# Performance work log

Measured on AMD Instinct MI355X. Metric: run time of the kernel, lower is better.

The kernel has to match this reference:

```python
import jax, jax.numpy as jnp
import numpy as np

CROSS_NUM, EXPERT_NUM, LOW_RANK = 3, 4, 64
BATCH, DIM = 32768, 512


def setup_inputs() -> dict:
    key = jax.random.key(0)
    ks = jax.random.split(key, 6)
    s = 0.05  # small init so tanh stays in its linear-ish range
    return {
        "x": jax.random.normal(ks[0], (BATCH, DIM), dtype=jnp.float32),
        "Vs": jax.random.normal(ks[1], (CROSS_NUM, EXPERT_NUM, LOW_RANK, DIM), dtype=jnp.float32) * s,
        "Cs": jax.random.normal(ks[2], (CROSS_NUM, EXPERT_NUM, LOW_RANK, LOW_RANK), dtype=jnp.float32) * s,
        "Us": jax.random.normal(ks[3], (CROSS_NUM, EXPERT_NUM, DIM, LOW_RANK), dtype=jnp.float32) * s,
        "bias": jax.random.normal(ks[4], (CROSS_NUM, DIM), dtype=jnp.float32) * s,
        "gate_w": jax.random.normal(ks[5], (DIM, EXPERT_NUM), dtype=jnp.float32) * s,
    }


def reference(x, Vs, Cs, Us, bias, gate_w):
    # x: [B, D]. The original keeps a trailing singleton axis; we drop it and
    # batch the per-expert einsum chain over the expert axis e.
    x0 = x
    x_l = x
    for i in range(CROSS_NUM):
        # gating (shared Dense(1) per expert, applied to current x_l): [B, E]
        g = x_l @ gate_w
        # low-rank expert chain, batched over experts
        v = jnp.tanh(jnp.einsum('eld,bd->bel', Vs[i], x_l))   # [B, E, low]
        c = jnp.tanh(jnp.einsum('elk,bek->bel', Cs[i], v))    # [B, E, low]
        u = jnp.einsum('edl,bel->bed', Us[i], c)              # [B, E, D]
        expert_out = (u + bias[i][None, None, :]) * x0[:, None, :]  # [B, E, D]
        # mixture combine (raw gating scores, no softmax, as in original)
        moe = jnp.einsum('bed,be->bd', expert_out, g)
        x_l = moe + x_l
    return x_l
```

## Files before the change

### kernel.cpp

```cpp
#include <hip/hip_runtime.h>
#include <hip/hip_bf16.h>


#define CROSS   3
#define ENUM    4
#define LR      64
#define ELD     256
#define DIM     512
#define BATCH   32768
#define BT      32
#define MT      2
#define NTHR    512

#define XL_W    520
#define Y_W     264

typedef __bf16 bf16x8 __attribute__((ext_vector_type(8)));
typedef float  f32x4  __attribute__((ext_vector_type(4)));
typedef unsigned short us;
typedef unsigned short us4 __attribute__((ext_vector_type(4)));

__device__ __forceinline__ us f2bf(float f) {
    return __builtin_bit_cast(us, (__bf16)f);
}
__device__ __forceinline__ float bf2f(us b) {
    unsigned int u = ((unsigned int)b) << 16;
    return __builtin_bit_cast(float, u);
}
__device__ __forceinline__ float tanh_fast(float x) {
    float t = __expf(2.f * x);
    return (t - 1.f) * __builtin_amdgcn_rcpf(t + 1.f);
}

#define MFMA(a, b, c) __builtin_amdgcn_mfma_f32_16x16x32_bf16(a, b, c, 0, 0, 0)

__global__ __launch_bounds__(64) void swz_all(
    const float* __restrict__ Vs, const float* __restrict__ Cs,
    const float* __restrict__ Us, const float* __restrict__ gw,
    us* __restrict__ Vf, us* __restrict__ Cf,
    us* __restrict__ Uf, us* __restrict__ Gf)
{
    int b = blockIdx.x;
    int lane = threadIdx.x;
    if (b < 768) {
        int i = b >> 8, t = b & 255;
        int nt = t >> 4, ks = t & 15;
        int n  = nt * 16 + (lane & 15);
        int k0 = ks * 32 + (lane >> 4) * 8;
        const float* src = Vs + (size_t)i * ELD * DIM + (size_t)n * DIM + k0;
        us* dst = Vf + (size_t)i * ELD * DIM
                + ((size_t)(nt * 16 + ks) * 64 + lane) * 8;
        #pragma unroll
        for (int j = 0; j < 8; ++j) dst[j] = f2bf(src[j]);
    } else if (b < 1536) {
        int bb = b - 768;
        int i = bb >> 8, t = bb & 255;
        int nt = t >> 3, ks = t & 7;
        int n  = nt * 16 + (lane & 15);
        int k0 = ks * 32 + (lane >> 4) * 8;
        int e = k0 >> 6, l0 = k0 & 63;
        const float* src = Us + (size_t)i * ENUM * DIM * LR
                         + (size_t)e * DIM * LR + (size_t)n * LR + l0;
        us* dst = Uf + (size_t)i * DIM * ELD
                + ((size_t)(nt * 8 + ks) * 64 + lane) * 8;
        #pragma unroll
        for (int j = 0; j < 8; ++j) dst[j] = f2bf(src[j]);
    } else if (b < 1632) {
        int bb = b - 1536;
        int i = bb >> 5, rest = bb & 31;
        int e = rest >> 3, t = rest & 7;
        int nt = t >> 1, ks = t & 1;
        int n  = nt * 16 + (lane & 15);
        int k0 = ks * 32 + (lane >> 4) * 8;
        const float* src = Cs + (((size_t)(i * ENUM + e) * LR + n) * LR) + k0;
        us* dst = Cf + (size_t)i * ENUM * LR * LR
                + ((size_t)((e * 4 + nt) * 2 + ks) * 64 + lane) * 8;
        #pragma unroll
        for (int j = 0; j < 8; ++j) dst[j] = f2bf(src[j]);
    } else {
        int ks = b - 1632;
        int n  = lane & 15;
        int k0 = ks * 32 + (lane >> 4) * 8;
        us* dst = Gf + ((size_t)ks * 64 + lane) * 8;
        #pragma unroll
        for (int j = 0; j < 8; ++j)
            dst[j] = (n < ENUM) ? f2bf(gw[(size_t)(k0 + j) * ENUM + n]) : (us)0;
    }
}

__global__ __launch_bounds__(NTHR, 6) void dcn_fused(
    const float* __restrict__ x,
    float* __restrict__ out,
    const us* __restrict__ Vf,
    const us* __restrict__ Cf,
    const us* __restrict__ Uf,
    const us* __restrict__ Gf,
    const float* __restrict__ bias)
{
    __shared__ us xl_s[BT * XL_W];
    __shared__ us y_s[BT * Y_W];
    __shared__ float g_s[BT * ENUM];

    const int tid  = threadIdx.x;
    const int wave = tid >> 6, lane = tid & 63;
    const int quad = lane >> 4, nl = lane & 15;
    const int row0 = blockIdx.x * BT;

    #pragma unroll
    for (int it = 0; it < 8; ++it) {
        int f4 = tid + it * NTHR;
        int r = f4 >> 7, c4 = f4 & 127;
        float4 v = *reinterpret_cast<const float4*>(
            x + (size_t)(row0 + r) * DIM + c4 * 4);
        us4 p;
        p[0] = f2bf(v.x); p[1] = f2bf(v.y); p[2] = f2bf(v.z); p[3] = f2bf(v.w);
        *reinterpret_cast<us4*>(&xl_s[r * XL_W + c4 * 4]) = p;
    }
    __syncthreads();

    unsigned int x0p[MT][4][2];
    #pragma unroll
    for (int mt = 0; mt < MT; ++mt)
        #pragma unroll
        for (int nt = 0; nt < 4; ++nt) {
            int rb = mt * 16 + quad * 4;
            int col = wave * 64 + nt * 16 + nl;
            unsigned int b0 = xl_s[(rb + 0) * XL_W + col];
            unsigned int b1 = xl_s[(rb + 1) * XL_W + col];
            unsigned int b2 = xl_s[(rb + 2) * XL_W + col];
            unsigned int b3 = xl_s[(rb + 3) * XL_W + col];
            x0p[mt][nt][0] = b0 | (b1 << 16);
            x0p[mt][nt][1] = b2 | (b3 << 16);
        }

    #pragma unroll 1
    for (int layer = 0; layer < CROSS; ++layer) {
        const us* Vl = Vf + (size_t)layer * ELD * DIM;
        const us* Cl = Cf + (size_t)layer * ENUM * LR * LR;
        const us* Ul = Uf + (size_t)layer * DIM * ELD;
        const float* bl = bias + layer * DIM;

        f32x4 acc1[MT][2];
        f32x4 gacc[MT];
        #pragma unroll
        for (int mt = 0; mt < MT; ++mt) {
            gacc[mt] = (f32x4)0.f;
            acc1[mt][0] = (f32x4)0.f;
            acc1[mt][1] = (f32x4)0.f;
        }
        #pragma unroll 4
        for (int ks = 0; ks < 16; ++ks) {
            bf16x8 a[MT];
            #pragma unroll
            for (int mt = 0; mt < MT; ++mt)
                a[mt] = *reinterpret_cast<const bf16x8*>(
                    &xl_s[(mt * 16 + nl) * XL_W + ks * 32 + quad * 8]);
            #pragma unroll
            for (int nt = 0; nt < 2; ++nt) {
                bf16x8 bfr = *reinterpret_cast<const bf16x8*>(
                    &Vl[((size_t)((wave * 2 + nt) * 16 + ks) * 64 + lane) * 8]);
                #pragma unroll
                for (int mt = 0; mt < MT; ++mt)
                    acc1[mt][nt] = MFMA(a[mt], bfr, acc1[mt][nt]);
            }
            if (wave == 0) {
                bf16x8 bg = *reinterpret_cast<const bf16x8*>(
                    &Gf[((size_t)ks * 64 + lane) * 8]);
                #pragma unroll
                for (int mt = 0; mt < MT; ++mt)
                    gacc[mt] = MFMA(a[mt], bg, gacc[mt]);
            }
        }
        #pragma unroll
        for (int mt = 0; mt < MT; ++mt)
            #pragma unroll
            for (int r = 0; r < 4; ++r) {
                int row = mt * 16 + quad * 4 + r;
                #pragma unroll
                for (int nt = 0; nt < 2; ++nt)
                    y_s[row * Y_W + wave * 32 + nt * 16 + nl] =
                        f2bf(tanh_fast(acc1[mt][nt][r]));
            }
        if (wave == 0 && nl < ENUM) {
            #pragma unroll
            for (int mt = 0; mt < MT; ++mt)
                #pragma unroll
                for (int r = 0; r < 4; ++r)
                    g_s[(mt * 16 + quad * 4 + r) * ENUM + nl] = gacc[mt][r];
        }
        __syncthreads();

        const int e = wave >> 1, h = wave & 1;
        f32x4 acc2[MT][2];
        #pragma unroll
        for (int mt = 0; mt < MT; ++mt) {
            acc2[mt][0] = (f32x4)0.f;
            acc2[mt][1] = (f32x4)0.f;
        }
        #pragma unroll
        for (int ks = 0; ks < 2; ++ks) {
            bf16x8 a[MT];
            #pragma unroll
            for (int mt = 0; mt < MT; ++mt)
                a[mt] = *reinterpret_cast<const bf16x8*>(
                    &y_s[(mt * 16 + nl) * Y_W + e * 64 + ks * 32 + quad * 8]);
            #pragma unroll
            for (int nt = 0; nt < 2; ++nt) {
                bf16x8 bfr = *reinterpret_cast<const bf16x8*>(
                    &Cl[((size_t)((e * 4 + h * 2 + nt) * 2 + ks) * 64 + lane) * 8]);
                #pragma unroll
                for (int mt = 0; mt < MT; ++mt)
                    acc2[mt][nt] = MFMA(a[mt], bfr, acc2[mt][nt]);
            }
        }
        __syncthreads();
        #pragma unroll
        for (int mt = 0; mt < MT; ++mt)
            #pragma unroll
            for (int r = 0; r < 4; ++r) {
                int row = mt * 16 + quad * 4 + r;
                float gv = g_s[row * ENUM + e];
                #pragma unroll
                for (int nt = 0; nt < 2; ++nt)
                    y_s[row * Y_W + e * 64 + h * 32 + nt * 16 + nl] =
                        f2bf(tanh_fast(acc2[mt][nt][r]) * gv);
            }
        __syncthreads();

        float Gv[MT][4];
        #pragma unroll
        for (int mt = 0; mt < MT; ++mt)
            #pragma unroll
            for (int r = 0; r < 4; ++r) {
                int row = mt * 16 + quad * 4 + r;
                f32x4 g4 = *reinterpret_cast<const f32x4*>(&g_s[row * ENUM]);
                Gv[mt][r] = g4[0] + g4[1] + g4[2] + g4[3];
            }

        #pragma unroll 1
        for (int h3 = 0; h3 < 2; ++h3) {
            float bc[2];
            bc[0] = bl[wave * 64 + h3 * 32 + nl];
            bc[1] = bl[wave * 64 + h3 * 32 + 16 + nl];
            f32x4 acc3[MT][2];
            #pragma unroll
            for (int mt = 0; mt < MT; ++mt) {
                acc3[mt][0] = (f32x4)0.f;
                acc3[mt][1] = (f32x4)0.f;
            }
            #pragma unroll 2
            for (int ks = 0; ks < 8; ++ks) {
                bf16x8 a[MT];
                #pragma unroll
                for (int mt = 0; mt < MT; ++mt)
                    a[mt] = *reinterpret_cast<const bf16x8*>(
                        &y_s[(mt * 16 + nl) * Y_W + ks * 32 + quad * 8]);
                #pragma unroll
                for (int nt = 0; nt < 2; ++nt) {
                    bf16x8 bfr = *reinterpret_cast<const bf16x8*>(
                        &Ul[((size_t)((wave * 4 + h3 * 2 + nt) * 8 + ks) * 64
                             + lane) * 8]);
                    #pragma unroll
                    for (int mt = 0; mt < MT; ++mt)
                        acc3[mt][nt] = MFMA(a[mt], bfr, acc3[mt][nt]);
                }
            }

            #pragma unroll
            for (int nt = 0; nt < 2; ++nt) {
                int col = wave * 64 + h3 * 32 + nt * 16 + nl;
                #pragma unroll
                for (int mt = 0; mt < MT; ++mt)
                    #pragma unroll
                    for (int r = 0; r < 4; ++r) {
                        int row = mt * 16 + quad * 4 + r;
                        float x0v = bf2f((us)(
                            x0p[mt][h3 * 2 + nt][r >> 1] >> ((r & 1) * 16)));
                        float xlo = bf2f(xl_s[row * XL_W + col]);
                        float res = xlo
                                  + x0v * (acc3[mt][nt][r] + bc[nt] * Gv[mt][r]);
                        if (layer == CROSS - 1)
                            out[(size_t)(row0 + row) * DIM + col] = res;
                        else
                            xl_s[row * XL_W + col] = f2bf(res);
                    }
            }
        }
        if (layer < CROSS - 1) __syncthreads();
    }
}

extern "C" void kernel_launch(void* const* d_in, const int* in_sizes, int n_in,
                              void* d_out, int out_size, void* d_ws,
                              size_t ws_size, hipStream_t stream) {
    const float* x      = (const float*)d_in[0];
    const float* Vs     = (const float*)d_in[1];
    const float* Cs     = (const float*)d_in[2];
    const float* Us     = (const float*)d_in[3];
    const float* bias   = (const float*)d_in[4];
    const float* gate_w = (const float*)d_in[5];
    float* out = (float*)d_out;

    us* Vf = (us*)d_ws;
    us* Uf = Vf + (size_t)CROSS * ELD * DIM;
    us* Cf = Uf + (size_t)CROSS * DIM * ELD;
    us* Gf = Cf + (size_t)CROSS * ENUM * LR * LR;

    swz_all<<<1648, 64, 0, stream>>>(Vs, Cs, Us, gate_w, Vf, Cf, Uf, Gf);
    dcn_fused<<<BATCH / BT, NTHR, 0, stream>>>(x, out, Vf, Cf, Uf, Gf, bias);
}
```

Baseline: 334.6 us.

## Double-buffer expert activations to drop a barrier and widen U-GEMM tile

Adds a second LDS buffer so the tanh(C·v)·g results go to z_s instead of overwriting y_s, which removes one __syncthreads between the C-GEMM reads and the writes. The U-projection loop is restructured so each wave computes all four 16-column tiles in a single pass with full unrolling, instead of two halves. The layer-1 K loop unroll is also raised. The wider accumulator set and extra LDS lower the occupancy hint from 6 to 4 waves per EU and may add register pressure.

```diff
diff --git a/kernel.cpp b/kernel.cpp
--- a/kernel.cpp
+++ b/kernel.cpp
@@ -88,7 +88,7 @@
     }
 }
 
-__global__ __launch_bounds__(NTHR, 6) void dcn_fused(
+__global__ __launch_bounds__(NTHR, 4) void dcn_fused(
     const float* __restrict__ x,
     float* __restrict__ out,
     const us* __restrict__ Vf,
@@ -99,6 +99,7 @@
 {
     __shared__ us xl_s[BT * XL_W];
     __shared__ us y_s[BT * Y_W];
+    __shared__ us z_s[BT * Y_W];
     __shared__ float g_s[BT * ENUM];
 
     const int tid  = threadIdx.x;
@@ -148,7 +149,7 @@
             acc1[mt][0] = (f32x4)0.f;
             acc1[mt][1] = (f32x4)0.f;
         }
-        #pragma unroll 4
+        #pragma unroll 8
         for (int ks = 0; ks < 16; ++ks) {
             bf16x8 a[MT];
             #pragma unroll
@@ -213,7 +214,6 @@
                     acc2[mt][nt] = MFMA(a[mt], bfr, acc2[mt][nt]);
             }
         }
-        __syncthreads();
         #pragma unroll
         for (int mt = 0; mt < MT; ++mt)
             #pragma unroll
@@ -222,7 +222,7 @@
                 float gv = g_s[row * ENUM + e];
                 #pragma unroll
                 for (int nt = 0; nt < 2; ++nt)
-                    y_s[row * Y_W + e * 64 + h * 32 + nt * 16 + nl] =
+                    z_s[row * Y_W + e * 64 + h * 32 + nt * 16 + nl] =
                         f2bf(tanh_fast(acc2[mt][nt][r]) * gv);
             }
         __syncthreads();
@@ -237,54 +237,47 @@
                 Gv[mt][r] = g4[0] + g4[1] + g4[2] + g4[3];
             }
 
-        #pragma unroll 1
-        for (int h3 = 0; h3 < 2; ++h3) {
-            float bc[2];
-            bc[0] = bl[wave * 64 + h3 * 32 + nl];
-            bc[1] = bl[wave * 64 + h3 * 32 + 16 + nl];
-            f32x4 acc3[MT][2];
-            #pragma unroll
-            for (int mt = 0; mt < MT; ++mt) {
-                acc3[mt][0] = (f32x4)0.f;
-                acc3[mt][1] = (f32x4)0.f;
-            }
-            #pragma unroll 2
-            for (int ks = 0; ks < 8; ++ks) {
-                bf16x8 a[MT];
+        f32x4 acc3[MT][4];
+        #pragma unroll
+        for (int mt = 0; mt < MT; ++mt)
+            #pragma unroll
+            for (int nt = 0; nt < 4; ++nt) acc3[mt][nt] = (f32x4)0.f;
+        #pragma unroll
+        for (int ks = 0; ks < 8; ++ks) {
+            bf16x8 a[MT];
+            #pragma unroll
+            for (int mt = 0; mt < MT; ++mt)
+                a[mt] = *reinterpret_cast<const bf16x8*>(
+                    &z_s[(mt * 16 + nl) * Y_W + ks * 32 + quad * 8]);
+            #pragma unroll
+            for (int nt = 0; nt < 4; ++nt) {
+                bf16x8 bfr = *reinterpret_cast<const bf16x8*>(
+                    &Ul[((size_t)((wave * 4 + nt) * 8 + ks) * 64 + lane) * 8]);
                 #pragma unroll
                 for (int mt = 0; mt < MT; ++mt)
-                    a[mt] = *reinterpret_cast<const bf16x8*>(
-                        &y_s[(mt * 16 + nl) * Y_W + ks * 32 + quad * 8]);
-                #pragma unroll
-                for (int nt = 0; nt < 2; ++nt) {
-                    bf16x8 bfr = *reinterpret_cast<const bf16x8*>(
-                        &Ul[((size_t)((wave * 4 + h3 * 2 + nt) * 8 + ks) * 64
-                             + lane) * 8]);
-                    #pragma unroll
-                    for (int mt = 0; mt < MT; ++mt)
-                        acc3[mt][nt] = MFMA(a[mt], bfr, acc3[mt][nt]);
+                    acc3[mt][nt] = MFMA(a[mt], bfr, acc3[mt][nt]);
+            }
+        }
+
+        #pragma unroll
+        for (int nt = 0; nt < 4; ++nt) {
+            int col = wave * 64 + nt * 16 + nl;
+            float bc = bl[col];
+            #pragma unroll
+            for (int mt = 0; mt < MT; ++mt)
+                #pragma unroll
+                for (int r = 0; r < 4; ++r) {
+                    int row = mt * 16 + quad * 4 + r;
+                    float x0v = bf2f(
+                        (us)(x0p[mt][nt][r >> 1] >> ((r & 1) * 16)));
+                    float xlo = bf2f(xl_s[row * XL_W + col]);
+                    float res = xlo
+                              + x0v * (acc3[mt][nt][r] + bc * Gv[mt][r]);
+                    if (layer == CROSS - 1)
+                        out[(size_t)(row0 + row) * DIM + col] = res;
+                    else
+                        xl_s[row * XL_W + col] = f2bf(res);
                 }
-            }
-
-            #pragma unroll
-            for (int nt = 0; nt < 2; ++nt) {
-                int col = wave * 64 + h3 * 32 + nt * 16 + nl;
-                #pragma unroll
-                for (int mt = 0; mt < MT; ++mt)
-                    #pragma unroll
-                    for (int r = 0; r < 4; ++r) {
-                        int row = mt * 16 + quad * 4 + r;
-                        float x0v = bf2f((us)(
-                            x0p[mt][h3 * 2 + nt][r >> 1] >> ((r & 1) * 16)));
-                        float xlo = bf2f(xl_s[row * XL_W + col]);
-                        float res = xlo
-                                  + x0v * (acc3[mt][nt][r] + bc[nt] * Gv[mt][r]);
-                        if (layer == CROSS - 1)
-                            out[(size_t)(row0 + row) * DIM + col] = res;
-                        else
-                            xl_s[row * XL_W + col] = f2bf(res);
-                    }
-            }
         }
         if (layer < CROSS - 1) __syncthreads();
     }
```

After: 367.9 us. 9.9% more time.
